# Performance work log

Hardware: AMD Instinct MI355X
Metric: run time of the kernel (lower is better)

The kernel has to match this reference:

```python
import jax, jax.numpy as jnp
import numpy as np

N_NODES = 50000
N_EDGES = 400000
D = 512
LN_EPS = 1e-5


def setup_inputs() -> dict:
    key = jax.random.key(0)
    k0, k1, k2, k3 = jax.random.split(key, 4)
    x = jax.random.normal(k0, (N_NODES, D), dtype=jnp.float32)
    src = jax.random.randint(k1, (N_EDGES,), 0, N_NODES, dtype=jnp.int64)
    dst = jax.random.randint(k2, (N_EDGES,), 0, N_NODES, dtype=jnp.int64)
    W = jax.random.normal(k3, (D, D), dtype=jnp.float32) * 0.05
    b = jnp.zeros((D,), dtype=jnp.float32)
    gamma = jnp.ones((D,), dtype=jnp.float32)
    beta = jnp.zeros((D,), dtype=jnp.float32)
    return {"x": x, "W": W, "b": b, "gamma": gamma, "beta": beta, "src": src, "dst": dst}


def reference(x, W, b, gamma, beta, src, dst):
    n = x.shape[0]
    ones = jnp.ones(src.shape, dtype=x.dtype)
    # DGL GraphConv norm='both': clamp degrees to >= 1
    deg_out = jnp.clip(jax.ops.segment_sum(ones, src, num_segments=n), 1.0)  # [N]
    deg_in = jnp.clip(jax.ops.segment_sum(ones, dst, num_segments=n), 1.0)   # [N]
    h = x * jax.lax.rsqrt(deg_out)[:, None]                 # [N, D] src normalization
    agg = jax.ops.segment_sum(h[src], dst, num_segments=n)  # gather->scatter-add SpMM
    h = agg * jax.lax.rsqrt(deg_in)[:, None]                # dst normalization
    h = h @ W + b                                           # dense linear
    # LayerNorm over last dim
    mu = jnp.mean(h, axis=-1, keepdims=True)
    var = jnp.mean(jnp.square(h - mu), axis=-1, keepdims=True)
    h = (h - mu) * jax.lax.rsqrt(var + LN_EPS) * gamma + beta
    # torch nn.GELU default = exact erf GELU
    return jax.nn.gelu(h, approximate=False)
```

## Files before the change

kernel.cpp:

```cpp
#include <hip/hip_runtime.h>
#include <hip/hip_bf16.h>

#define D 512

typedef __attribute__((ext_vector_type(8))) short bf16x8;
typedef __attribute__((ext_vector_type(4))) float f32x4;

__device__ inline float b2f(short h) {
    union { unsigned u; float f; } c;
    c.u = ((unsigned)(unsigned short)h) << 16;
    return c.f;
}

__global__ void k_hist(const int* __restrict__ src, const int* __restrict__ dst,
                       int* __restrict__ deg_out, int* __restrict__ deg_in, int E) {
    int e = blockIdx.x * 256 + threadIdx.x;
    if (e < E) {
        atomicAdd(&deg_out[src[e]], 1);
        atomicAdd(&deg_in[dst[e]], 1);
    }
}

__global__ __launch_bounds__(256)
void k_scale(const float* __restrict__ x, const int* __restrict__ deg_out,
             __hip_bfloat16* __restrict__ xs, int total16) {
    int i = blockIdx.x * 256 + threadIdx.x;
    if (i >= total16) return;
    int node = i >> 6;
    float w = rsqrtf((float)max(deg_out[node], 1));
    const float4* p = (const float4*)(x + (size_t)i * 8);
    float4 a = p[0], b = p[1];
    union { float4 f4; __hip_bfloat16 h[8]; } o;
    o.h[0] = __float2bfloat16(a.x * w);
    o.h[1] = __float2bfloat16(a.y * w);
    o.h[2] = __float2bfloat16(a.z * w);
    o.h[3] = __float2bfloat16(a.w * w);
    o.h[4] = __float2bfloat16(b.x * w);
    o.h[5] = __float2bfloat16(b.y * w);
    o.h[6] = __float2bfloat16(b.z * w);
    o.h[7] = __float2bfloat16(b.w * w);
    *(float4*)(xs + (size_t)i * 8) = o.f4;
}

__global__ void k_scan1(const int* __restrict__ deg_in, int* __restrict__ row_start,
                        int* __restrict__ partials, int N) {
    __shared__ int sm[1024];
    int tid = threadIdx.x;
    int i = blockIdx.x * 1024 + tid;
    int v = (i < N) ? deg_in[i] : 0;
    sm[tid] = v;
    __syncthreads();
    int acc = v;
    #pragma unroll
    for (int off = 1; off < 1024; off <<= 1) {
        int t = (tid >= off) ? sm[tid - off] : 0;
        __syncthreads();
        acc += t;
        sm[tid] = acc;
        __syncthreads();
    }
    if (i < N) row_start[i] = acc - v;
    if (tid == 1023) partials[blockIdx.x] = acc;
}

__global__ void k_scan2w(int* __restrict__ partials, int* __restrict__ row_start,
                         int nb, int N) {
    int lane = threadIdx.x;
    int orig = (lane < nb) ? partials[lane] : 0;
    int v = orig;
    #pragma unroll
    for (int off = 1; off < 64; off <<= 1) {
        int t = __shfl_up(v, off, 64);
        if (lane >= off) v += t;
    }
    if (lane < nb) partials[lane] = v - orig;
    if (lane == 63) row_start[N] = v;
}

__global__ void k_scan2s(int* __restrict__ partials, int* __restrict__ row_start,
                         int nb, int N) {
    if (threadIdx.x == 0 && blockIdx.x == 0) {
        int run = 0;
        for (int b = 0; b < nb; b++) { int t = partials[b]; partials[b] = run; run += t; }
        row_start[N] = run;
    }
}

__global__ void k_scan3(int* __restrict__ row_start, const int* __restrict__ partials, int N) {
    int i = blockIdx.x * 256 + threadIdx.x;
    if (i < N) row_start[i] += partials[i >> 10];
}

__global__ void k_fill(const int* __restrict__ src, const int* __restrict__ dst,
                       const int* __restrict__ row_start, int* __restrict__ cursor,
                       int* __restrict__ csr_src, int E) {
    int e = blockIdx.x * 256 + threadIdx.x;
    if (e < E) {
        int d = dst[e];
        int slot = atomicAdd(&cursor[d], 1);
        csr_src[row_start[d] + slot] = src[e];
    }
}

__global__ __launch_bounds__(1024)
void k_spmm(const __hip_bfloat16* __restrict__ xs, const int* __restrict__ row_start,
            const int* __restrict__ csr_src, __hip_bfloat16* __restrict__ Ap, int N) {
    int wid = threadIdx.x >> 6;
    int lane = threadIdx.x & 63;
    int node = blockIdx.x * 16 + wid;
    if (node >= N) return;
    int rs = row_start[node], re = row_start[node + 1];

    float acc[8];
    #pragma unroll
    for (int k = 0; k < 8; k++) acc[k] = 0.f;
    const __hip_bfloat16* xl = xs + (size_t)lane * 8;

    int j = rs;
    for (; j + 4 <= re; j += 4) {
        int s0 = csr_src[j], s1 = csr_src[j + 1], s2 = csr_src[j + 2], s3 = csr_src[j + 3];
        bf16x8 v0 = *(const bf16x8*)(xl + (size_t)s0 * D);
        bf16x8 v1 = *(const bf16x8*)(xl + (size_t)s1 * D);
        bf16x8 v2 = *(const bf16x8*)(xl + (size_t)s2 * D);
        bf16x8 v3 = *(const bf16x8*)(xl + (size_t)s3 * D);
        #pragma unroll
        for (int k = 0; k < 8; k++)
            acc[k] += (b2f(v0[k]) + b2f(v1[k])) + (b2f(v2[k]) + b2f(v3[k]));
    }
    for (; j < re; j++) {
        int s = csr_src[j];
        bf16x8 v = *(const bf16x8*)(xl + (size_t)s * D);
        #pragma unroll
        for (int k = 0; k < 8; k++) acc[k] += b2f(v[k]);
    }

    float rn = rsqrtf((float)max(re - rs, 1));
    union { float4 f4; __hip_bfloat16 h[8]; } o;
    #pragma unroll
    for (int k = 0; k < 8; k++) o.h[k] = __float2bfloat16(acc[k] * rn);
    *(float4*)((char*)Ap + ((size_t)(node >> 4) * 1024 + lane * 16 + (node & 15)) * 16) = o.f4;
}

__global__ __launch_bounds__(256)
void k_spmm_f32(const float* __restrict__ x, const int* __restrict__ row_start,
                const int* __restrict__ csr_src, const int* __restrict__ deg_out,
                __hip_bfloat16* __restrict__ A, int N) {
    int wid = threadIdx.x >> 6;
    int lane = threadIdx.x & 63;
    int node = blockIdx.x * 4 + wid;
    if (node >= N) return;
    int rs = row_start[node], re = row_start[node + 1];
    float4 acc0 = {0.f, 0.f, 0.f, 0.f};
    float4 acc1 = {0.f, 0.f, 0.f, 0.f};
    const float* xl = x + (size_t)lane * 8;
    for (int j = rs; j < re; j++) {
        int s = csr_src[j];
        float w = rsqrtf((float)max(deg_out[s], 1));
        const float4* p = (const float4*)(xl + (size_t)s * D);
        float4 a = p[0], b = p[1];
        acc0.x += a.x * w; acc0.y += a.y * w; acc0.z += a.z * w; acc0.w += a.w * w;
        acc1.x += b.x * w; acc1.y += b.y * w; acc1.z += b.z * w; acc1.w += b.w * w;
    }
    float rn = rsqrtf((float)max(re - rs, 1));
    union { float4 f4; __hip_bfloat16 h[8]; } o;
    o.h[0] = __float2bfloat16(acc0.x * rn);
    o.h[1] = __float2bfloat16(acc0.y * rn);
    o.h[2] = __float2bfloat16(acc0.z * rn);
    o.h[3] = __float2bfloat16(acc0.w * rn);
    o.h[4] = __float2bfloat16(acc1.x * rn);
    o.h[5] = __float2bfloat16(acc1.y * rn);
    o.h[6] = __float2bfloat16(acc1.z * rn);
    o.h[7] = __float2bfloat16(acc1.w * rn);
    *(float4*)(A + (size_t)node * D + lane * 8) = o.f4;
}

__global__ void k_packw2(const float* __restrict__ W, __hip_bfloat16* __restrict__ Wp) {
    int bid = blockIdx.x;
    int c = bid >> 7, kt = (bid >> 3) & 15, ntc = bid & 7;
    int lane = threadIdx.x;
    int k0 = kt * 32 + (lane >> 4) * 8;
    int n  = (c * 8 + ntc) * 16 + (lane & 15);
    union { float4 f4; __hip_bfloat16 h[8]; } o;
    #pragma unroll
    for (int j = 0; j < 8; j++)
        o.h[j] = __float2bfloat16(W[(size_t)(k0 + j) * D + n]);
    *(float4*)(Wp + ((size_t)bid * 64 + lane) * 8) = o.f4;
}

__global__ void k_packw(const float* __restrict__ W, __hip_bfloat16* __restrict__ Wp) {
    int tile = blockIdx.x;
    int lane = threadIdx.x;
    int kt = tile >> 5, nt = tile & 31;
    int k0 = kt * 32 + (lane >> 4) * 8;
    int n  = nt * 16 + (lane & 15);
    union { float4 f4; __hip_bfloat16 h[8]; } o;
    #pragma unroll
    for (int j = 0; j < 8; j++)
        o.h[j] = __float2bfloat16(W[(size_t)(k0 + j) * D + n]);
    *(float4*)(Wp + ((size_t)tile * 64 + lane) * 8) = o.f4;
}

__global__ __launch_bounds__(512, 4)
void k_gemm3(const __hip_bfloat16* __restrict__ Ap, const __hip_bfloat16* __restrict__ Wp,
             const float* __restrict__ bias, const float* __restrict__ gamma,
             const float* __restrict__ beta, float* __restrict__ out, int M) {
    __shared__ float s_sum[64][4];
    __shared__ float s_sq[64][4];

    int tid = threadIdx.x;
    int wid = tid >> 6, lane = tid & 63;
    int wm = wid >> 2, wn = wid & 3;
    int l4 = lane >> 4, coll = lane & 15;
    int tb = blockIdx.x * 64;
    int rgmax = ((M + 15) >> 4) - 1;

    int rg0 = (tb >> 4) + wm * 2;
    int rgA = min(rg0, rgmax);
    int rgB = min(rg0 + 1, rgmax);
    const char* a0 = (const char*)Ap + (size_t)rgA * 16384 + (size_t)lane * 16;
    const char* a1 = (const char*)Ap + (size_t)rgB * 16384 + (size_t)lane * 16;
    const char* wb = (const char*)Wp + ((size_t)(wn * 128) * 64 + lane) * 16;

    f32x4 acc0[8], acc1[8];
    #pragma unroll
    for (int t = 0; t < 8; t++) { acc0[t] = (f32x4){0,0,0,0}; acc1[t] = (f32x4){0,0,0,0}; }

    for (int kt = 0; kt < 16; kt++) {
        bf16x8 af0 = *(const bf16x8*)(a0 + (size_t)kt * 1024);
        bf16x8 af1 = *(const bf16x8*)(a1 + (size_t)kt * 1024);
        const char* wk = wb + (size_t)kt * 8192;
        #pragma unroll
        for (int t = 0; t < 8; t++) {
            bf16x8 bf = *(const bf16x8*)(wk + (size_t)t * 1024);
            acc0[t] = __builtin_amdgcn_mfma_f32_16x16x32_bf16(af0, bf, acc0[t], 0, 0, 0);
            acc1[t] = __builtin_amdgcn_mfma_f32_16x16x32_bf16(af1, bf, acc1[t], 0, 0, 0);
        }
    }

    float bia[8], gam[8], bet[8];
    #pragma unroll
    for (int t = 0; t < 8; t++) {
        int col = wn * 128 + t * 16 + coll;
        bia[t] = bias[col]; gam[t] = gamma[col]; bet[t] = beta[col];
    }
    #pragma unroll
    for (int ai = 0; ai < 2; ai++) {
        f32x4* acc = ai ? acc1 : acc0;
        #pragma unroll
        for (int r = 0; r < 4; r++) {
            float s = 0.f, q = 0.f;
            #pragma unroll
            for (int t = 0; t < 8; t++) {
                float v = acc[t][r] + bia[t];
                acc[t][r] = v;
                s += v; q += v * v;
            }
            #pragma unroll
            for (int off = 1; off < 16; off <<= 1) {
                s += __shfl_xor(s, off, 64);
                q += __shfl_xor(q, off, 64);
            }
            if (coll == 0) {
                int rb = wm * 32 + ai * 16 + l4 * 4 + r;
                s_sum[rb][wn] = s;
                s_sq[rb][wn] = q;
            }
        }
    }
    __syncthreads();

    #pragma unroll
    for (int ai = 0; ai < 2; ai++) {
        f32x4* acc = ai ? acc1 : acc0;
        #pragma unroll
        for (int r = 0; r < 4; r++) {
            int rb = wm * 32 + ai * 16 + l4 * 4 + r;
            int gr = tb + rb;
            if (gr >= M) continue;
            float s = s_sum[rb][0] + s_sum[rb][1] + s_sum[rb][2] + s_sum[rb][3];
            float q = s_sq[rb][0] + s_sq[rb][1] + s_sq[rb][2] + s_sq[rb][3];
            float mean = s * (1.0f / 512.0f);
            float var = q * (1.0f / 512.0f) - mean * mean;
            float rstd = rsqrtf(fmaxf(var, 0.f) + 1e-5f);
            float* orow = out + (size_t)gr * D + wn * 128 + coll;
            #pragma unroll
            for (int t = 0; t < 8; t++) {
                float y = (acc[t][r] - mean) * rstd * gam[t] + bet[t];
                float yy = y * y;
                float pz = fmaf(yy, -0.1029423374f, -2.3022076728f);
                float e = __builtin_amdgcn_exp2f(y * pz);
                float g = y * __builtin_amdgcn_rcpf(1.0f + e);
                orow[t * 16] = g;
            }
        }
    }
}

__global__ __launch_bounds__(512)
void k_gemm(const __hip_bfloat16* __restrict__ A, const __hip_bfloat16* __restrict__ Wp,
            const float* __restrict__ bias, const float* __restrict__ gamma,
            const float* __restrict__ beta, float* __restrict__ out, int M) {
    int tid = threadIdx.x;
    int wid = tid >> 6, lane = tid & 63;
    int wm = wid >> 2;
    int wn = wid & 3;
    int l4 = lane >> 4, coll = lane & 15;
    int m0 = blockIdx.x * 32 + wm * 16;
    int arow = m0 + coll;
    bool rowok = (arow < M);

    f32x4 acc[8];
    #pragma unroll
    for (int t = 0; t < 8; t++) acc[t] = (f32x4){0.f, 0.f, 0.f, 0.f};

    const bf16x8* wpb = (const bf16x8*)Wp;
    for (int kt = 0; kt < 16; kt++) {
        bf16x8 afrag;
        if (rowok) afrag = *(const bf16x8*)(A + (size_t)arow * D + kt * 32 + l4 * 8);
        else afrag = (bf16x8){0,0,0,0,0,0,0,0};
        const bf16x8* wp = wpb + ((size_t)(kt * 32 + wn * 8) * 64 + lane);
        #pragma unroll
        for (int t = 0; t < 8; t++) {
            bf16x8 bfrag = wp[(size_t)t * 64];
            acc[t] = __builtin_amdgcn_mfma_f32_16x16x32_bf16(afrag, bfrag, acc[t], 0, 0, 0);
        }
    }
    __shared__ float s_sum[32][4];
    __shared__ float s_sq[32][4];
    #pragma unroll
    for (int r = 0; r < 4; r++) {
        float s = 0.f, q = 0.f;
        #pragma unroll
        for (int t = 0; t < 8; t++) {
            int col = wn * 128 + t * 16 + coll;
            float v = acc[t][r] + bias[col];
            acc[t][r] = v;
            s += v; q += v * v;
        }
        #pragma unroll
        for (int off = 1; off < 16; off <<= 1) {
            s += __shfl_xor(s, off, 64);
            q += __shfl_xor(q, off, 64);
        }
        if (coll == 0) {
            int rb = wm * 16 + l4 * 4 + r;
            s_sum[rb][wn] = s;
            s_sq[rb][wn] = q;
        }
    }
    __syncthreads();
    #pragma unroll
    for (int r = 0; r < 4; r++) {
        int rb = wm * 16 + l4 * 4 + r;
        int gr = blockIdx.x * 32 + rb;
        if (gr >= M) continue;
        float s = s_sum[rb][0] + s_sum[rb][1] + s_sum[rb][2] + s_sum[rb][3];
        float q = s_sq[rb][0] + s_sq[rb][1] + s_sq[rb][2] + s_sq[rb][3];
        float mean = s * (1.0f / 512.0f);
        float var = q * (1.0f / 512.0f) - mean * mean;
        float rstd = rsqrtf(fmaxf(var, 0.f) + 1e-5f);
        #pragma unroll
        for (int t = 0; t < 8; t++) {
            int col = wn * 128 + t * 16 + coll;
            float y = (acc[t][r] - mean) * rstd * gamma[col] + beta[col];
            float yy = y * y;
            float pz = fmaf(yy, -0.1029423374f, -2.3022076728f);
            float e = __builtin_amdgcn_exp2f(y * pz);
            out[(size_t)gr * D + col] = y * __builtin_amdgcn_rcpf(1.0f + e);
        }
    }
}

extern "C" void kernel_launch(void* const* d_in, const int* in_sizes, int n_in,
                              void* d_out, int out_size, void* d_ws, size_t ws_size,
                              hipStream_t stream) {
    const float* x     = (const float*)d_in[0];
    const float* W     = (const float*)d_in[1];
    const float* b     = (const float*)d_in[2];
    const float* gamma = (const float*)d_in[3];
    const float* beta  = (const float*)d_in[4];
    const int*   src   = (const int*)d_in[5];
    const int*   dst   = (const int*)d_in[6];
    int N = in_sizes[0] / D;
    int E = in_sizes[5];
    float* out = (float*)d_out;

    int* deg_out   = (int*)d_ws;
    int* deg_in    = deg_out + N;
    int* row_start = deg_in + N;
    int* cursor    = row_start + N + 1;
    int* partials  = cursor + N;
    int* csr_src   = partials + 64;
    uintptr_t p = (uintptr_t)(csr_src + E);
    p = (p + 255) & ~(uintptr_t)255;
    __hip_bfloat16* A = (__hip_bfloat16*)p;
    p += (size_t)(((N + 15) / 16) * 16) * D * sizeof(__hip_bfloat16);
    p = (p + 255) & ~(uintptr_t)255;
    __hip_bfloat16* Wp = (__hip_bfloat16*)p;
    p += (size_t)D * D * sizeof(__hip_bfloat16);
    p = (p + 255) & ~(uintptr_t)255;
    __hip_bfloat16* xs = (__hip_bfloat16*)p;
    size_t need_xs = (p - (uintptr_t)d_ws) + (size_t)N * D * sizeof(__hip_bfloat16);
    bool use_bf16_path = (ws_size >= need_xs);

    hipMemsetAsync(deg_out, 0, (size_t)2 * N * sizeof(int), stream);
    hipMemsetAsync(cursor, 0, (size_t)N * sizeof(int), stream);

    k_hist<<<(E + 255) / 256, 256, 0, stream>>>(src, dst, deg_out, deg_in, E);
    int nb1 = (N + 1023) / 1024;
    k_scan1<<<nb1, 1024, 0, stream>>>(deg_in, row_start, partials, N);
    if (nb1 <= 64)
        k_scan2w<<<1, 64, 0, stream>>>(partials, row_start, nb1, N);
    else
        k_scan2s<<<1, 64, 0, stream>>>(partials, row_start, nb1, N);
    k_scan3<<<(N + 255) / 256, 256, 0, stream>>>(row_start, partials, N);
    k_fill<<<(E + 255) / 256, 256, 0, stream>>>(src, dst, row_start, cursor, csr_src, E);

    if (use_bf16_path) {
        int total16 = N * 64;
        k_scale<<<(total16 + 255) / 256, 256, 0, stream>>>(x, deg_out, xs, total16);
        k_spmm<<<(N + 15) / 16, 1024, 0, stream>>>(xs, row_start, csr_src, A, N);
        k_packw2<<<512, 64, 0, stream>>>(W, Wp);
        k_gemm3<<<(N + 63) / 64, 512, 0, stream>>>(A, Wp, b, gamma, beta, out, N);
    } else {
        k_spmm_f32<<<(N + 3) / 4, 256, 0, stream>>>(x, row_start, csr_src, deg_out, A, N);
        k_packw<<<512, 64, 0, stream>>>(W, Wp);
        k_gemm<<<(N + 31) / 32, 512, 0, stream>>>(A, Wp, b, gamma, beta, out, N);
    }
}
```

Baseline: 240.6 us.

## Use row-major A with 128-row GEMM tiles reusing W fragments across four row groups

The SpMM now writes the aggregated features row-major instead of in a packed 16-row MFMA layout, and runs with 256-thread blocks. The fused GEMM+LayerNorm+GELU kernel doubles its row tile to 128, so each wave holds four A fragments and reuses each loaded W fragment across four MFMAs, cutting W reloads per output. The cost is higher register pressure (occupancy hint dropped to 2), A loads that are strided by row rather than contiguous packed tiles, and fewer blocks in the grid.

```diff
diff --git a/kernel.cpp b/kernel.cpp
--- a/kernel.cpp
+++ b/kernel.cpp
@@ -102,12 +102,12 @@
     }
 }
 
-__global__ __launch_bounds__(1024)
+__global__ __launch_bounds__(256)
 void k_spmm(const __hip_bfloat16* __restrict__ xs, const int* __restrict__ row_start,
-            const int* __restrict__ csr_src, __hip_bfloat16* __restrict__ Ap, int N) {
+            const int* __restrict__ csr_src, __hip_bfloat16* __restrict__ A, int N) {
     int wid = threadIdx.x >> 6;
     int lane = threadIdx.x & 63;
-    int node = blockIdx.x * 16 + wid;
+    int node = blockIdx.x * 4 + wid;
     if (node >= N) return;
     int rs = row_start[node], re = row_start[node + 1];
 
@@ -138,7 +138,7 @@
     union { float4 f4; __hip_bfloat16 h[8]; } o;
     #pragma unroll
     for (int k = 0; k < 8; k++) o.h[k] = __float2bfloat16(acc[k] * rn);
-    *(float4*)((char*)Ap + ((size_t)(node >> 4) * 1024 + lane * 16 + (node & 15)) * 16) = o.f4;
+    *(float4*)(A + (size_t)node * D + lane * 8) = o.f4;
 }
 
 __global__ __launch_bounds__(256)
@@ -200,41 +200,49 @@
     *(float4*)(Wp + ((size_t)tile * 64 + lane) * 8) = o.f4;
 }
 
-__global__ __launch_bounds__(512, 4)
-void k_gemm3(const __hip_bfloat16* __restrict__ Ap, const __hip_bfloat16* __restrict__ Wp,
+__global__ __launch_bounds__(512, 2)
+void k_gemm4(const __hip_bfloat16* __restrict__ A, const __hip_bfloat16* __restrict__ Wp,
              const float* __restrict__ bias, const float* __restrict__ gamma,
              const float* __restrict__ beta, float* __restrict__ out, int M) {
-    __shared__ float s_sum[64][4];
-    __shared__ float s_sq[64][4];
+    __shared__ float s_sum[128][4];
+    __shared__ float s_sq[128][4];
 
     int tid = threadIdx.x;
     int wid = tid >> 6, lane = tid & 63;
     int wm = wid >> 2, wn = wid & 3;
     int l4 = lane >> 4, coll = lane & 15;
-    int tb = blockIdx.x * 64;
-    int rgmax = ((M + 15) >> 4) - 1;
-
-    int rg0 = (tb >> 4) + wm * 2;
-    int rgA = min(rg0, rgmax);
-    int rgB = min(rg0 + 1, rgmax);
-    const char* a0 = (const char*)Ap + (size_t)rgA * 16384 + (size_t)lane * 16;
-    const char* a1 = (const char*)Ap + (size_t)rgB * 16384 + (size_t)lane * 16;
+    int tb = blockIdx.x * 128;
+
+    const char* ap[4];
+    #pragma unroll
+    for (int ai = 0; ai < 4; ai++) {
+        int row = tb + wm * 64 + ai * 16 + coll;
+        if (row > M - 1) row = M - 1;
+        ap[ai] = (const char*)A + (size_t)row * 1024 + l4 * 16;
+    }
     const char* wb = (const char*)Wp + ((size_t)(wn * 128) * 64 + lane) * 16;
 
-    f32x4 acc0[8], acc1[8];
-    #pragma unroll
-    for (int t = 0; t < 8; t++) { acc0[t] = (f32x4){0,0,0,0}; acc1[t] = (f32x4){0,0,0,0}; }
+    f32x4 acc[4][8];
+    #pragma unroll
+    for (int ai = 0; ai < 4; ai++)
+        #pragma unroll
+        for (int t = 0; t < 8; t++) acc[ai][t] = (f32x4){0.f, 0.f, 0.f, 0.f};
 
     for (int kt = 0; kt < 16; kt++) {
-        bf16x8 af0 = *(const bf16x8*)(a0 + (size_t)kt * 1024);
-        bf16x8 af1 = *(const bf16x8*)(a1 + (size_t)kt * 1024);
+        bf16x8 af[4];
+        #pragma unroll
+        for (int ai = 0; ai < 4; ai++)
+            af[ai] = *(const bf16x8*)(ap[ai] + (size_t)kt * 64);
         const char* wk = wb + (size_t)kt * 8192;
-        #pragma unroll
-        for (int t = 0; t < 8; t++) {
-            bf16x8 bf = *(const bf16x8*)(wk + (size_t)t * 1024);
-            acc0[t] = __builtin_amdgcn_mfma_f32_16x16x32_bf16(af0, bf, acc0[t], 0, 0, 0);
-            acc1[t] = __builtin_amdgcn_mfma_f32_16x16x32_bf16(af1, bf, acc1[t], 0, 0, 0);
-        }
+        bf16x8 bf[8];
+        #pragma unroll
+        for (int t = 0; t < 8; t++)
+            bf[t] = *(const bf16x8*)(wk + (size_t)t * 1024);
+        #pragma unroll
+        for (int t = 0; t < 8; t++)
+            #pragma unroll
+            for (int ai = 0; ai < 4; ai++)
+                acc[ai][t] = __builtin_amdgcn_mfma_f32_16x16x32_bf16(af[ai], bf[t], acc[ai][t], 0, 0, 0);
     }
 
     float bia[8], gam[8], bet[8];
@@ -244,15 +252,14 @@
         bia[t] = bias[col]; gam[t] = gamma[col]; bet[t] = beta[col];
     }
     #pragma unroll
-    for (int ai = 0; ai < 2; ai++) {
-        f32x4* acc = ai ? acc1 : acc0;
+    for (int ai = 0; ai < 4; ai++) {
         #pragma unroll
         for (int r = 0; r < 4; r++) {
             float s = 0.f, q = 0.f;
             #pragma unroll
             for (int t = 0; t < 8; t++) {
-                float v = acc[t][r] + bia[t];
-                acc[t][r] = v;
+                float v = acc[ai][t][r] + bia[t];
+                acc[ai][t][r] = v;
                 s += v; q += v * v;
             }
             #pragma unroll
@@ -261,7 +268,7 @@
                 q += __shfl_xor(q, off, 64);
             }
             if (coll == 0) {
-                int rb = wm * 32 + ai * 16 + l4 * 4 + r;
+                int rb = wm * 64 + ai * 16 + l4 * 4 + r;
                 s_sum[rb][wn] = s;
                 s_sq[rb][wn] = q;
             }
@@ -270,11 +277,10 @@
     __syncthreads();
 
     #pragma unroll
-    for (int ai = 0; ai < 2; ai++) {
-        f32x4* acc = ai ? acc1 : acc0;
+    for (int ai = 0; ai < 4; ai++) {
         #pragma unroll
         for (int r = 0; r < 4; r++) {
-            int rb = wm * 32 + ai * 16 + l4 * 4 + r;
+            int rb = wm * 64 + ai * 16 + l4 * 4 + r;
             int gr = tb + rb;
             if (gr >= M) continue;
             float s = s_sum[rb][0] + s_sum[rb][1] + s_sum[rb][2] + s_sum[rb][3];
@@ -285,7 +291,7 @@
             float* orow = out + (size_t)gr * D + wn * 128 + coll;
             #pragma unroll
             for (int t = 0; t < 8; t++) {
-                float y = (acc[t][r] - mean) * rstd * gam[t] + bet[t];
+                float y = (acc[ai][t][r] - mean) * rstd * gam[t] + bet[t];
                 float yy = y * y;
                 float pz = fmaf(yy, -0.1029423374f, -2.3022076728f);
                 float e = __builtin_amdgcn_exp2f(y * pz);
@@ -394,7 +400,7 @@
     uintptr_t p = (uintptr_t)(csr_src + E);
     p = (p + 255) & ~(uintptr_t)255;
     __hip_bfloat16* A = (__hip_bfloat16*)p;
-    p += (size_t)(((N + 15) / 16) * 16) * D * sizeof(__hip_bfloat16);
+    p += (size_t)N * D * sizeof(__hip_bfloat16);
     p = (p + 255) & ~(uintptr_t)255;
     __hip_bfloat16* Wp = (__hip_bfloat16*)p;
     p += (size_t)D * D * sizeof(__hip_bfloat16);
@@ -419,9 +425,9 @@
     if (use_bf16_path) {
         int total16 = N * 64;
         k_scale<<<(total16 + 255) / 256, 256, 0, stream>>>(x, deg_out, xs, total16);
-        k_spmm<<<(N + 15) / 16, 1024, 0, stream>>>(xs, row_start, csr_src, A, N);
+        k_spmm<<<(N + 3) / 4, 256, 0, stream>>>(xs, row_start, csr_src, A, N);
         k_packw2<<<512, 64, 0, stream>>>(W, Wp);
-        k_gemm3<<<(N + 63) / 64, 512, 0, stream>>>(A, Wp, b, gamma, beta, out, N);
+        k_gemm4<<<(N + 127) / 128, 512, 0, stream>>>(A, Wp, b, gamma, beta, out, N);
     } else {
         k_spmm_f32<<<(N + 3) / 4, 256, 0, stream>>>(x, row_start, csr_src, deg_out, A, N);
         k_packw<<<512, 64, 0, stream>>>(W, Wp);
```

Measured after the change: 250.9 us. 4.3% more time.

## Fuse SpMM aggregation into GEMM+LayerNorm kernel via swizzled LDS tile

Applied to the files above, without the earlier changes.

The separate SpMM kernel is removed. Each GEMM block now gathers and aggregates its own 64 destination rows into a 64KB XOR-swizzled shared-memory tile, then runs the MFMA GEMM with the LayerNorm/GELU epilogue reading A from LDS. This avoids writing the aggregated bf16 matrix to global memory, reading it back, and paying one kernel launch. In exchange, 64KB of LDS per block caps occupancy at two blocks per CU, and the gather phase and MFMA phase can no longer overlap across kernels.

```diff
diff --git a/kernel.cpp b/kernel.cpp
--- a/kernel.cpp
+++ b/kernel.cpp
@@ -102,43 +102,152 @@
     }
 }
 
-__global__ __launch_bounds__(1024)
-void k_spmm(const __hip_bfloat16* __restrict__ xs, const int* __restrict__ row_start,
-            const int* __restrict__ csr_src, __hip_bfloat16* __restrict__ Ap, int N) {
-    int wid = threadIdx.x >> 6;
-    int lane = threadIdx.x & 63;
-    int node = blockIdx.x * 16 + wid;
-    if (node >= N) return;
-    int rs = row_start[node], re = row_start[node + 1];
-
-    float acc[8];
-    #pragma unroll
-    for (int k = 0; k < 8; k++) acc[k] = 0.f;
-    const __hip_bfloat16* xl = xs + (size_t)lane * 8;
-
-    int j = rs;
-    for (; j + 4 <= re; j += 4) {
-        int s0 = csr_src[j], s1 = csr_src[j + 1], s2 = csr_src[j + 2], s3 = csr_src[j + 3];
-        bf16x8 v0 = *(const bf16x8*)(xl + (size_t)s0 * D);
-        bf16x8 v1 = *(const bf16x8*)(xl + (size_t)s1 * D);
-        bf16x8 v2 = *(const bf16x8*)(xl + (size_t)s2 * D);
-        bf16x8 v3 = *(const bf16x8*)(xl + (size_t)s3 * D);
-        #pragma unroll
-        for (int k = 0; k < 8; k++)
-            acc[k] += (b2f(v0[k]) + b2f(v1[k])) + (b2f(v2[k]) + b2f(v3[k]));
-    }
-    for (; j < re; j++) {
-        int s = csr_src[j];
-        bf16x8 v = *(const bf16x8*)(xl + (size_t)s * D);
-        #pragma unroll
-        for (int k = 0; k < 8; k++) acc[k] += b2f(v[k]);
-    }
-
-    float rn = rsqrtf((float)max(re - rs, 1));
+__global__ void k_packw2(const float* __restrict__ W, __hip_bfloat16* __restrict__ Wp) {
+    int bid = blockIdx.x;
+    int c = bid >> 7, kt = (bid >> 3) & 15, ntc = bid & 7;
+    int lane = threadIdx.x;
+    int k0 = kt * 32 + (lane >> 4) * 8;
+    int n  = (c * 8 + ntc) * 16 + (lane & 15);
     union { float4 f4; __hip_bfloat16 h[8]; } o;
     #pragma unroll
-    for (int k = 0; k < 8; k++) o.h[k] = __float2bfloat16(acc[k] * rn);
-    *(float4*)((char*)Ap + ((size_t)(node >> 4) * 1024 + lane * 16 + (node & 15)) * 16) = o.f4;
+    for (int j = 0; j < 8; j++)
+        o.h[j] = __float2bfloat16(W[(size_t)(k0 + j) * D + n]);
+    *(float4*)(Wp + ((size_t)bid * 64 + lane) * 8) = o.f4;
+}
+
+__global__ __launch_bounds__(512, 2)
+void k_fused(const __hip_bfloat16* __restrict__ xs, const int* __restrict__ row_start,
+             const int* __restrict__ csr_src, const __hip_bfloat16* __restrict__ Wp,
+             const float* __restrict__ bias, const float* __restrict__ gamma,
+             const float* __restrict__ beta, float* __restrict__ out, int M) {
+    __shared__ __align__(16) char ldsA[65536];
+    __shared__ float s_sum[64][4];
+    __shared__ float s_sq[64][4];
+
+    int tid = threadIdx.x;
+    int wid = tid >> 6, lane = tid & 63;
+    int l4 = lane >> 4, coll = lane & 15;
+    int tb = blockIdx.x * 64;
+
+    {
+        const __hip_bfloat16* xl = xs + (size_t)lane * 8;
+        for (int i = 0; i < 8; i++) {
+            int rowt = wid * 8 + i;
+            int node = tb + rowt;
+            char* dst = ldsA + rowt * 1024 + ((lane * 16) ^ ((rowt & 7) << 4));
+            if (node < M) {
+                int rs = row_start[node], re = row_start[node + 1];
+                float acc[8];
+                #pragma unroll
+                for (int k = 0; k < 8; k++) acc[k] = 0.f;
+                int j = rs;
+                for (; j + 4 <= re; j += 4) {
+                    int s0 = csr_src[j], s1 = csr_src[j + 1], s2 = csr_src[j + 2], s3 = csr_src[j + 3];
+                    bf16x8 v0 = *(const bf16x8*)(xl + (size_t)s0 * D);
+                    bf16x8 v1 = *(const bf16x8*)(xl + (size_t)s1 * D);
+                    bf16x8 v2 = *(const bf16x8*)(xl + (size_t)s2 * D);
+                    bf16x8 v3 = *(const bf16x8*)(xl + (size_t)s3 * D);
+                    #pragma unroll
+                    for (int k = 0; k < 8; k++)
+                        acc[k] += (b2f(v0[k]) + b2f(v1[k])) + (b2f(v2[k]) + b2f(v3[k]));
+                }
+                for (; j < re; j++) {
+                    int s = csr_src[j];
+                    bf16x8 v = *(const bf16x8*)(xl + (size_t)s * D);
+                    #pragma unroll
+                    for (int k = 0; k < 8; k++) acc[k] += b2f(v[k]);
+                }
+                float rn = rsqrtf((float)max(re - rs, 1));
+                union { float4 f4; __hip_bfloat16 h[8]; } o;
+                #pragma unroll
+                for (int k = 0; k < 8; k++) o.h[k] = __float2bfloat16(acc[k] * rn);
+                *(float4*)dst = o.f4;
+            } else {
+                *(float4*)dst = (float4){0.f, 0.f, 0.f, 0.f};
+            }
+        }
+    }
+    __syncthreads();
+
+    int wm = wid >> 2, wn = wid & 3;
+    int r0 = wm * 32 + coll;
+    int r1 = r0 + 16;
+    const char* wb = (const char*)Wp + ((size_t)(wn * 128) * 64 + lane) * 16;
+
+    f32x4 acc0[8], acc1[8];
+    #pragma unroll
+    for (int t = 0; t < 8; t++) { acc0[t] = (f32x4){0,0,0,0}; acc1[t] = (f32x4){0,0,0,0}; }
+
+    for (int kt = 0; kt < 16; kt++) {
+        int kb = kt * 64 + l4 * 16;
+        bf16x8 af0 = *(const bf16x8*)(ldsA + r0 * 1024 + (kb ^ ((r0 & 7) << 4)));
+        bf16x8 af1 = *(const bf16x8*)(ldsA + r1 * 1024 + (kb ^ ((r1 & 7) << 4)));
+        const char* wk = wb + (size_t)kt * 8192;
+        #pragma unroll
+        for (int t = 0; t < 8; t++) {
+            bf16x8 bf = *(const bf16x8*)(wk + (size_t)t * 1024);
+            acc0[t] = __builtin_amdgcn_mfma_f32_16x16x32_bf16(af0, bf, acc0[t], 0, 0, 0);
+            acc1[t] = __builtin_amdgcn_mfma_f32_16x16x32_bf16(af1, bf, acc1[t], 0, 0, 0);
+        }
+    }
+
+    float bia[8], gam[8], bet[8];
+    #pragma unroll
+    for (int t = 0; t < 8; t++) {
+        int col = wn * 128 + t * 16 + coll;
+        bia[t] = bias[col]; gam[t] = gamma[col]; bet[t] = beta[col];
+    }
+    #pragma unroll
+    for (int ai = 0; ai < 2; ai++) {
+        f32x4* acc = ai ? acc1 : acc0;
+        #pragma unroll
+        for (int r = 0; r < 4; r++) {
+            float s = 0.f, q = 0.f;
+            #pragma unroll
+            for (int t = 0; t < 8; t++) {
+                float v = acc[t][r] + bia[t];
+                acc[t][r] = v;
+                s += v; q += v * v;
+            }
+            #pragma unroll
+            for (int off = 1; off < 16; off <<= 1) {
+                s += __shfl_xor(s, off, 64);
+                q += __shfl_xor(q, off, 64);
+            }
+            if (coll == 0) {
+                int rb = wm * 32 + ai * 16 + l4 * 4 + r;
+                s_sum[rb][wn] = s;
+                s_sq[rb][wn] = q;
+            }
+        }
+    }
+    __syncthreads();
+
+    #pragma unroll
+    for (int ai = 0; ai < 2; ai++) {
+        f32x4* acc = ai ? acc1 : acc0;
+        #pragma unroll
+        for (int r = 0; r < 4; r++) {
+            int rb = wm * 32 + ai * 16 + l4 * 4 + r;
+            int gr = tb + rb;
+            if (gr >= M) continue;
+            float s = s_sum[rb][0] + s_sum[rb][1] + s_sum[rb][2] + s_sum[rb][3];
+            float q = s_sq[rb][0] + s_sq[rb][1] + s_sq[rb][2] + s_sq[rb][3];
+            float mean = s * (1.0f / 512.0f);
+            float var = q * (1.0f / 512.0f) - mean * mean;
+            float rstd = rsqrtf(fmaxf(var, 0.f) + 1e-5f);
+            float* orow = out + (size_t)gr * D + wn * 128 + coll;
+            #pragma unroll
+            for (int t = 0; t < 8; t++) {
+                float y = (acc[t][r] - mean) * rstd * gam[t] + bet[t];
+                float yy = y * y;
+                float pz = fmaf(yy, -0.1029423374f, -2.3022076728f);
+                float e = __builtin_amdgcn_exp2f(y * pz);
+                float g = y * __builtin_amdgcn_rcpf(1.0f + e);
+                orow[t * 16] = g;
+            }
+        }
+    }
 }
 
 __global__ __launch_bounds__(256)
@@ -174,19 +283,6 @@
     *(float4*)(A + (size_t)node * D + lane * 8) = o.f4;
 }
 
-__global__ void k_packw2(const float* __restrict__ W, __hip_bfloat16* __restrict__ Wp) {
-    int bid = blockIdx.x;
-    int c = bid >> 7, kt = (bid >> 3) & 15, ntc = bid & 7;
-    int lane = threadIdx.x;
-    int k0 = kt * 32 + (lane >> 4) * 8;
-    int n  = (c * 8 + ntc) * 16 + (lane & 15);
-    union { float4 f4; __hip_bfloat16 h[8]; } o;
-    #pragma unroll
-    for (int j = 0; j < 8; j++)
-        o.h[j] = __float2bfloat16(W[(size_t)(k0 + j) * D + n]);
-    *(float4*)(Wp + ((size_t)bid * 64 + lane) * 8) = o.f4;
-}
-
 __global__ void k_packw(const float* __restrict__ W, __hip_bfloat16* __restrict__ Wp) {
     int tile = blockIdx.x;
     int lane = threadIdx.x;
@@ -198,102 +294,6 @@
     for (int j = 0; j < 8; j++)
         o.h[j] = __float2bfloat16(W[(size_t)(k0 + j) * D + n]);
     *(float4*)(Wp + ((size_t)tile * 64 + lane) * 8) = o.f4;
-}
-
-__global__ __launch_bounds__(512, 4)
-void k_gemm3(const __hip_bfloat16* __restrict__ Ap, const __hip_bfloat16* __restrict__ Wp,
-             const float* __restrict__ bias, const float* __restrict__ gamma,
-             const float* __restrict__ beta, float* __restrict__ out, int M) {
-    __shared__ float s_sum[64][4];
-    __shared__ float s_sq[64][4];
-
-    int tid = threadIdx.x;
-    int wid = tid >> 6, lane = tid & 63;
-    int wm = wid >> 2, wn = wid & 3;
-    int l4 = lane >> 4, coll = lane & 15;
-    int tb = blockIdx.x * 64;
-    int rgmax = ((M + 15) >> 4) - 1;
-
-    int rg0 = (tb >> 4) + wm * 2;
-    int rgA = min(rg0, rgmax);
-    int rgB = min(rg0 + 1, rgmax);
-    const char* a0 = (const char*)Ap + (size_t)rgA * 16384 + (size_t)lane * 16;
-    const char* a1 = (const char*)Ap + (size_t)rgB * 16384 + (size_t)lane * 16;
-    const char* wb = (const char*)Wp + ((size_t)(wn * 128) * 64 + lane) * 16;
-
-    f32x4 acc0[8], acc1[8];
-    #pragma unroll
-    for (int t = 0; t < 8; t++) { acc0[t] = (f32x4){0,0,0,0}; acc1[t] = (f32x4){0,0,0,0}; }
-
-    for (int kt = 0; kt < 16; kt++) {
-        bf16x8 af0 = *(const bf16x8*)(a0 + (size_t)kt * 1024);
-        bf16x8 af1 = *(const bf16x8*)(a1 + (size_t)kt * 1024);
-        const char* wk = wb + (size_t)kt * 8192;
-        #pragma unroll
-        for (int t = 0; t < 8; t++) {
-            bf16x8 bf = *(const bf16x8*)(wk + (size_t)t * 1024);
-            acc0[t] = __builtin_amdgcn_mfma_f32_16x16x32_bf16(af0, bf, acc0[t], 0, 0, 0);
-            acc1[t] = __builtin_amdgcn_mfma_f32_16x16x32_bf16(af1, bf, acc1[t], 0, 0, 0);
-        }
-    }
-
-    float bia[8], gam[8], bet[8];
-    #pragma unroll
-    for (int t = 0; t < 8; t++) {
-        int col = wn * 128 + t * 16 + coll;
-        bia[t] = bias[col]; gam[t] = gamma[col]; bet[t] = beta[col];
-    }
-    #pragma unroll
-    for (int ai = 0; ai < 2; ai++) {
-        f32x4* acc = ai ? acc1 : acc0;
-        #pragma unroll
-        for (int r = 0; r < 4; r++) {
-            float s = 0.f, q = 0.f;
-            #pragma unroll
-            for (int t = 0; t < 8; t++) {
-                float v = acc[t][r] + bia[t];
-                acc[t][r] = v;
-                s += v; q += v * v;
-            }
-            #pragma unroll
-            for (int off = 1; off < 16; off <<= 1) {
-                s += __shfl_xor(s, off, 64);
-                q += __shfl_xor(q, off, 64);
-            }
-            if (coll == 0) {
-                int rb = wm * 32 + ai * 16 + l4 * 4 + r;
-                s_sum[rb][wn] = s;
-                s_sq[rb][wn] = q;
-            }
-        }
-    }
-    __syncthreads();
-
-    #pragma unroll
-    for (int ai = 0; ai < 2; ai++) {
-        f32x4* acc = ai ? acc1 : acc0;
-        #pragma unroll
-        for (int r = 0; r < 4; r++) {
-            int rb = wm * 32 + ai * 16 + l4 * 4 + r;
-            int gr = tb + rb;
-            if (gr >= M) continue;
-            float s = s_sum[rb][0] + s_sum[rb][1] + s_sum[rb][2] + s_sum[rb][3];
-            float q = s_sq[rb][0] + s_sq[rb][1] + s_sq[rb][2] + s_sq[rb][3];
-            float mean = s * (1.0f / 512.0f);
-            float var = q * (1.0f / 512.0f) - mean * mean;
-            float rstd = rsqrtf(fmaxf(var, 0.f) + 1e-5f);
-            float* orow = out + (size_t)gr * D + wn * 128 + coll;
-            #pragma unroll
-            for (int t = 0; t < 8; t++) {
-                float y = (acc[t][r] - mean) * rstd * gam[t] + bet[t];
-                float yy = y * y;
-                float pz = fmaf(yy, -0.1029423374f, -2.3022076728f);
-                float e = __builtin_amdgcn_exp2f(y * pz);
-                float g = y * __builtin_amdgcn_rcpf(1.0f + e);
-                orow[t * 16] = g;
-            }
-        }
-    }
 }
 
 __global__ __launch_bounds__(512)
@@ -394,7 +394,7 @@
     uintptr_t p = (uintptr_t)(csr_src + E);
     p = (p + 255) & ~(uintptr_t)255;
     __hip_bfloat16* A = (__hip_bfloat16*)p;
-    p += (size_t)(((N + 15) / 16) * 16) * D * sizeof(__hip_bfloat16);
+    p += (size_t)N * D * sizeof(__hip_bfloat16);
     p = (p + 255) & ~(uintptr_t)255;
     __hip_bfloat16* Wp = (__hip_bfloat16*)p;
     p += (size_t)D * D * sizeof(__hip_bfloat16);
@@ -419,9 +419,9 @@
     if (use_bf16_path) {
         int total16 = N * 64;
         k_scale<<<(total16 + 255) / 256, 256, 0, stream>>>(x, deg_out, xs, total16);
-        k_spmm<<<(N + 15) / 16, 1024, 0, stream>>>(xs, row_start, csr_src, A, N);
         k_packw2<<<512, 64, 0, stream>>>(W, Wp);
-        k_gemm3<<<(N + 63) / 64, 512, 0, stream>>>(A, Wp, b, gamma, beta, out, N);
+        k_fused<<<(N + 63) / 64, 512, 0, stream>>>(xs, row_start, csr_src, Wp,
+                                                   b, gamma, beta, out, N);
     } else {
         k_spmm_f32<<<(N + 3) / 4, 256, 0, stream>>>(x, row_start, csr_src, deg_out, A, N);
         k_packw<<<512, 64, 0, stream>>>(W, Wp);
```

After: 291.4 us. 21.1% more time.

## Fuse degree scan with x scaling and seed cursor with row offsets

Applied to the files above, without the earlier changes.

Replaces the three-stage multi-kernel prefix scan with a single-block scan that runs in block 0 of a new kernel, while the remaining 256 blocks scale x to bf16 in a grid-stride loop. The cursor array is initialised to the row offsets, so the fill kernel writes directly to the atomic slot and the separate cursor memset and row_start read are dropped. This removes several launches and a memset. In exchange the scan is serialised in one block, which may become the critical path, and the scale pass now runs on fewer blocks.

```diff
diff --git a/kernel.cpp b/kernel.cpp
--- a/kernel.cpp
+++ b/kernel.cpp
@@ -21,84 +21,70 @@
     }
 }
 
-__global__ __launch_bounds__(256)
-void k_scale(const float* __restrict__ x, const int* __restrict__ deg_out,
-             __hip_bfloat16* __restrict__ xs, int total16) {
-    int i = blockIdx.x * 256 + threadIdx.x;
-    if (i >= total16) return;
-    int node = i >> 6;
-    float w = rsqrtf((float)max(deg_out[node], 1));
-    const float4* p = (const float4*)(x + (size_t)i * 8);
-    float4 a = p[0], b = p[1];
-    union { float4 f4; __hip_bfloat16 h[8]; } o;
-    o.h[0] = __float2bfloat16(a.x * w);
-    o.h[1] = __float2bfloat16(a.y * w);
-    o.h[2] = __float2bfloat16(a.z * w);
-    o.h[3] = __float2bfloat16(a.w * w);
-    o.h[4] = __float2bfloat16(b.x * w);
-    o.h[5] = __float2bfloat16(b.y * w);
-    o.h[6] = __float2bfloat16(b.z * w);
-    o.h[7] = __float2bfloat16(b.w * w);
-    *(float4*)(xs + (size_t)i * 8) = o.f4;
-}
-
-__global__ void k_scan1(const int* __restrict__ deg_in, int* __restrict__ row_start,
-                        int* __restrict__ partials, int N) {
-    __shared__ int sm[1024];
-    int tid = threadIdx.x;
-    int i = blockIdx.x * 1024 + tid;
-    int v = (i < N) ? deg_in[i] : 0;
-    sm[tid] = v;
-    __syncthreads();
-    int acc = v;
-    #pragma unroll
-    for (int off = 1; off < 1024; off <<= 1) {
-        int t = (tid >= off) ? sm[tid - off] : 0;
+__global__ __launch_bounds__(1024)
+void k_scale_scan(const float* __restrict__ x, const int* __restrict__ deg_out,
+                  const int* __restrict__ deg_in, __hip_bfloat16* __restrict__ xs,
+                  int* __restrict__ row_start, int* __restrict__ cursor,
+                  int N, int total16, int do_scale) {
+    if (blockIdx.x == 0) {
+        __shared__ int sm[1024];
+        int tid = threadIdx.x;
+        int per = (N + 1023) >> 10;
+        int base = tid * per;
+        int local = 0;
+        for (int i = 0; i < per; i++) {
+            int idx = base + i;
+            if (idx < N) local += deg_in[idx];
+        }
+        sm[tid] = local;
         __syncthreads();
-        acc += t;
-        sm[tid] = acc;
-        __syncthreads();
-    }
-    if (i < N) row_start[i] = acc - v;
-    if (tid == 1023) partials[blockIdx.x] = acc;
-}
-
-__global__ void k_scan2w(int* __restrict__ partials, int* __restrict__ row_start,
-                         int nb, int N) {
-    int lane = threadIdx.x;
-    int orig = (lane < nb) ? partials[lane] : 0;
-    int v = orig;
-    #pragma unroll
-    for (int off = 1; off < 64; off <<= 1) {
-        int t = __shfl_up(v, off, 64);
-        if (lane >= off) v += t;
-    }
-    if (lane < nb) partials[lane] = v - orig;
-    if (lane == 63) row_start[N] = v;
-}
-
-__global__ void k_scan2s(int* __restrict__ partials, int* __restrict__ row_start,
-                         int nb, int N) {
-    if (threadIdx.x == 0 && blockIdx.x == 0) {
-        int run = 0;
-        for (int b = 0; b < nb; b++) { int t = partials[b]; partials[b] = run; run += t; }
-        row_start[N] = run;
-    }
-}
-
-__global__ void k_scan3(int* __restrict__ row_start, const int* __restrict__ partials, int N) {
-    int i = blockIdx.x * 256 + threadIdx.x;
-    if (i < N) row_start[i] += partials[i >> 10];
+        int acc = local;
+        #pragma unroll
+        for (int off = 1; off < 1024; off <<= 1) {
+            int t = (tid >= off) ? sm[tid - off] : 0;
+            __syncthreads();
+            acc += t;
+            sm[tid] = acc;
+            __syncthreads();
+        }
+        int run = acc - local;
+        for (int i = 0; i < per; i++) {
+            int idx = base + i;
+            if (idx < N) {
+                row_start[idx] = run;
+                cursor[idx] = run;
+                run += deg_in[idx];
+            }
+        }
+        if (tid == 1023) row_start[N] = run;
+        return;
+    }
+    if (!do_scale) return;
+    int stride = (gridDim.x - 1) * 1024;
+    for (int i = (blockIdx.x - 1) * 1024 + threadIdx.x; i < total16; i += stride) {
+        int node = i >> 6;
+        float w = rsqrtf((float)max(deg_out[node], 1));
+        const float4* p = (const float4*)(x + (size_t)i * 8);
+        float4 a = p[0], b = p[1];
+        union { float4 f4; __hip_bfloat16 h[8]; } o;
+        o.h[0] = __float2bfloat16(a.x * w);
+        o.h[1] = __float2bfloat16(a.y * w);
+        o.h[2] = __float2bfloat16(a.z * w);
+        o.h[3] = __float2bfloat16(a.w * w);
+        o.h[4] = __float2bfloat16(b.x * w);
+        o.h[5] = __float2bfloat16(b.y * w);
+        o.h[6] = __float2bfloat16(b.z * w);
+        o.h[7] = __float2bfloat16(b.w * w);
+        *(float4*)(xs + (size_t)i * 8) = o.f4;
+    }
 }
 
 __global__ void k_fill(const int* __restrict__ src, const int* __restrict__ dst,
-                       const int* __restrict__ row_start, int* __restrict__ cursor,
-                       int* __restrict__ csr_src, int E) {
+                       int* __restrict__ cursor, int* __restrict__ csr_src, int E) {
     int e = blockIdx.x * 256 + threadIdx.x;
     if (e < E) {
-        int d = dst[e];
-        int slot = atomicAdd(&cursor[d], 1);
-        csr_src[row_start[d] + slot] = src[e];
+        int slot = atomicAdd(&cursor[dst[e]], 1);
+        csr_src[slot] = src[e];
     }
 }
 
@@ -139,6 +125,115 @@
     #pragma unroll
     for (int k = 0; k < 8; k++) o.h[k] = __float2bfloat16(acc[k] * rn);
     *(float4*)((char*)Ap + ((size_t)(node >> 4) * 1024 + lane * 16 + (node & 15)) * 16) = o.f4;
+}
+
+__global__ void k_packw2(const float* __restrict__ W, __hip_bfloat16* __restrict__ Wp) {
+    int bid = blockIdx.x;
+    int c = bid >> 7, kt = (bid >> 3) & 15, ntc = bid & 7;
+    int lane = threadIdx.x;
+    int k0 = kt * 32 + (lane >> 4) * 8;
+    int n  = (c * 8 + ntc) * 16 + (lane & 15);
+    union { float4 f4; __hip_bfloat16 h[8]; } o;
+    #pragma unroll
+    for (int j = 0; j < 8; j++)
+        o.h[j] = __float2bfloat16(W[(size_t)(k0 + j) * D + n]);
+    *(float4*)(Wp + ((size_t)bid * 64 + lane) * 8) = o.f4;
+}
+
+__global__ __launch_bounds__(512, 4)
+void k_gemm3(const __hip_bfloat16* __restrict__ Ap, const __hip_bfloat16* __restrict__ Wp,
+             const float* __restrict__ bias, const float* __restrict__ gamma,
+             const float* __restrict__ beta, float* __restrict__ out, int M) {
+    __shared__ float s_sum[64][4];
+    __shared__ float s_sq[64][4];
+
+    int tid = threadIdx.x;
+    int wid = tid >> 6, lane = tid & 63;
+    int wm = wid >> 2, wn = wid & 3;
+    int l4 = lane >> 4, coll = lane & 15;
+    int tb = blockIdx.x * 64;
+    int rgmax = ((M + 15) >> 4) - 1;
+
+    int rg0 = (tb >> 4) + wm * 2;
+    int rgA = min(rg0, rgmax);
+    int rgB = min(rg0 + 1, rgmax);
+    const char* a0 = (const char*)Ap + (size_t)rgA * 16384 + (size_t)lane * 16;
+    const char* a1 = (const char*)Ap + (size_t)rgB * 16384 + (size_t)lane * 16;
+    const char* wb = (const char*)Wp + ((size_t)(wn * 128) * 64 + lane) * 16;
+
+    f32x4 acc0[8], acc1[8];
+    #pragma unroll
+    for (int t = 0; t < 8; t++) { acc0[t] = (f32x4){0,0,0,0}; acc1[t] = (f32x4){0,0,0,0}; }
+
+    for (int kt = 0; kt < 16; kt++) {
+        bf16x8 af0 = *(const bf16x8*)(a0 + (size_t)kt * 1024);
+        bf16x8 af1 = *(const bf16x8*)(a1 + (size_t)kt * 1024);
+        const char* wk = wb + (size_t)kt * 8192;
+        #pragma unroll
+        for (int t = 0; t < 8; t++) {
+            bf16x8 bf = *(const bf16x8*)(wk + (size_t)t * 1024);
+            acc0[t] = __builtin_amdgcn_mfma_f32_16x16x32_bf16(af0, bf, acc0[t], 0, 0, 0);
+            acc1[t] = __builtin_amdgcn_mfma_f32_16x16x32_bf16(af1, bf, acc1[t], 0, 0, 0);
+        }
+    }
+
+    float bia[8], gam[8], bet[8];
+    #pragma unroll
+    for (int t = 0; t < 8; t++) {
+        int col = wn * 128 + t * 16 + coll;
+        bia[t] = bias[col]; gam[t] = gamma[col]; bet[t] = beta[col];
+    }
+    #pragma unroll
+    for (int ai = 0; ai < 2; ai++) {
+        f32x4* acc = ai ? acc1 : acc0;
+        #pragma unroll
+        for (int r = 0; r < 4; r++) {
+            float s = 0.f, q = 0.f;
+            #pragma unroll
+            for (int t = 0; t < 8; t++) {
+                float v = acc[t][r] + bia[t];
+                acc[t][r] = v;
+                s += v; q += v * v;
+            }
+            #pragma unroll
+            for (int off = 1; off < 16; off <<= 1) {
+                s += __shfl_xor(s, off, 64);
+                q += __shfl_xor(q, off, 64);
+            }
+            if (coll == 0) {
+                int rb = wm * 32 + ai * 16 + l4 * 4 + r;
+                s_sum[rb][wn] = s;
+                s_sq[rb][wn] = q;
+            }
+        }
+    }
+    __syncthreads();
+
+    #pragma unroll
+    for (int ai = 0; ai < 2; ai++) {
+        f32x4* acc = ai ? acc1 : acc0;
+        #pragma unroll
+        for (int r = 0; r < 4; r++) {
+            int rb = wm * 32 + ai * 16 + l4 * 4 + r;
+            int gr = tb + rb;
+            if (gr >= M) continue;
+            float s = s_sum[rb][0] + s_sum[rb][1] + s_sum[rb][2] + s_sum[rb][3];
+            float q = s_sq[rb][0] + s_sq[rb][1] + s_sq[rb][2] + s_sq[rb][3];
+            float mean = s * (1.0f / 512.0f);
+            float var = q * (1.0f / 512.0f) - mean * mean;
+            float rstd = rsqrtf(fmaxf(var, 0.f) + 1e-5f);
+            float* orow = out + (size_t)gr * D + wn * 128 + coll;
+            #pragma unroll
+            for (int t = 0; t < 8; t++) {
+                float y = (acc[t][r] - mean) * rstd * gam[t] + bet[t];
+                float yy = y * y;
+                float pz = fmaf(yy, -0.1029423374f, -2.3022076728f);
+                float e = __builtin_amdgcn_exp2f(y * pz);
+                float g = y * __builtin_amdgcn_rcpf(1.0f + e);
+                orow[t * 16] = g;
+            }
+        }
+    }
 }
 
 __global__ __launch_bounds__(256)
@@ -174,19 +269,6 @@
     *(float4*)(A + (size_t)node * D + lane * 8) = o.f4;
 }
 
-__global__ void k_packw2(const float* __restrict__ W, __hip_bfloat16* __restrict__ Wp) {
-    int bid = blockIdx.x;
-    int c = bid >> 7, kt = (bid >> 3) & 15, ntc = bid & 7;
-    int lane = threadIdx.x;
-    int k0 = kt * 32 + (lane >> 4) * 8;
-    int n  = (c * 8 + ntc) * 16 + (lane & 15);
-    union { float4 f4; __hip_bfloat16 h[8]; } o;
-    #pragma unroll
-    for (int j = 0; j < 8; j++)
-        o.h[j] = __float2bfloat16(W[(size_t)(k0 + j) * D + n]);
-    *(float4*)(Wp + ((size_t)bid * 64 + lane) * 8) = o.f4;
-}
-
 __global__ void k_packw(const float* __restrict__ W, __hip_bfloat16* __restrict__ Wp) {
     int tile = blockIdx.x;
     int lane = threadIdx.x;
@@ -198,102 +280,6 @@
     for (int j = 0; j < 8; j++)
         o.h[j] = __float2bfloat16(W[(size_t)(k0 + j) * D + n]);
     *(float4*)(Wp + ((size_t)tile * 64 + lane) * 8) = o.f4;
-}
-
-__global__ __launch_bounds__(512, 4)
-void k_gemm3(const __hip_bfloat16* __restrict__ Ap, const __hip_bfloat16* __restrict__ Wp,
-             const float* __restrict__ bias, const float* __restrict__ gamma,
-             const float* __restrict__ beta, float* __restrict__ out, int M) {
-    __shared__ float s_sum[64][4];
-    __shared__ float s_sq[64][4];
-
-    int tid = threadIdx.x;
-    int wid = tid >> 6, lane = tid & 63;
-    int wm = wid >> 2, wn = wid & 3;
-    int l4 = lane >> 4, coll = lane & 15;
-    int tb = blockIdx.x * 64;
-    int rgmax = ((M + 15) >> 4) - 1;
-
-    int rg0 = (tb >> 4) + wm * 2;
-    int rgA = min(rg0, rgmax);
-    int rgB = min(rg0 + 1, rgmax);
-    const char* a0 = (const char*)Ap + (size_t)rgA * 16384 + (size_t)lane * 16;
-    const char* a1 = (const char*)Ap + (size_t)rgB * 16384 + (size_t)lane * 16;
-    const char* wb = (const char*)Wp + ((size_t)(wn * 128) * 64 + lane) * 16;
-
-    f32x4 acc0[8], acc1[8];
-    #pragma unroll
-    for (int t = 0; t < 8; t++) { acc0[t] = (f32x4){0,0,0,0}; acc1[t] = (f32x4){0,0,0,0}; }
-
-    for (int kt = 0; kt < 16; kt++) {
-        bf16x8 af0 = *(const bf16x8*)(a0 + (size_t)kt * 1024);
-        bf16x8 af1 = *(const bf16x8*)(a1 + (size_t)kt * 1024);
-        const char* wk = wb + (size_t)kt * 8192;
-        #pragma unroll
-        for (int t = 0; t < 8; t++) {
-            bf16x8 bf = *(const bf16x8*)(wk + (size_t)t * 1024);
-            acc0[t] = __builtin_amdgcn_mfma_f32_16x16x32_bf16(af0, bf, acc0[t], 0, 0, 0);
-            acc1[t] = __builtin_amdgcn_mfma_f32_16x16x32_bf16(af1, bf, acc1[t], 0, 0, 0);
-        }
-    }
-
-    float bia[8], gam[8], bet[8];
-    #pragma unroll
-    for (int t = 0; t < 8; t++) {
-        int col = wn * 128 + t * 16 + coll;
-        bia[t] = bias[col]; gam[t] = gamma[col]; bet[t] = beta[col];
-    }
-    #pragma unroll
-    for (int ai = 0; ai < 2; ai++) {
-        f32x4* acc = ai ? acc1 : acc0;
-        #pragma unroll
-        for (int r = 0; r < 4; r++) {
-            float s = 0.f, q = 0.f;
-            #pragma unroll
-            for (int t = 0; t < 8; t++) {
-                float v = acc[t][r] + bia[t];
-                acc[t][r] = v;
-                s += v; q += v * v;
-            }
-            #pragma unroll
-            for (int off = 1; off < 16; off <<= 1) {
-                s += __shfl_xor(s, off, 64);
-                q += __shfl_xor(q, off, 64);
-            }
-            if (coll == 0) {
-                int rb = wm * 32 + ai * 16 + l4 * 4 + r;
-                s_sum[rb][wn] = s;
-                s_sq[rb][wn] = q;
-            }
-        }
-    }
-    __syncthreads();
-
-    #pragma unroll
-    for (int ai = 0; ai < 2; ai++) {
-        f32x4* acc = ai ? acc1 : acc0;
-        #pragma unroll
-        for (int r = 0; r < 4; r++) {
-            int rb = wm * 32 + ai * 16 + l4 * 4 + r;
-            int gr = tb + rb;
-            if (gr >= M) continue;
-            float s = s_sum[rb][0] + s_sum[rb][1] + s_sum[rb][2] + s_sum[rb][3];
-            float q = s_sq[rb][0] + s_sq[rb][1] + s_sq[rb][2] + s_sq[rb][3];
-            float mean = s * (1.0f / 512.0f);
-            float var = q * (1.0f / 512.0f) - mean * mean;
-            float rstd = rsqrtf(fmaxf(var, 0.f) + 1e-5f);
-            float* orow = out + (size_t)gr * D + wn * 128 + coll;
-            #pragma unroll
-            for (int t = 0; t < 8; t++) {
-                float y = (acc[t][r] - mean) * rstd * gam[t] + bet[t];
-                float yy = y * y;
-                float pz = fmaf(yy, -0.1029423374f, -2.3022076728f);
-                float e = __builtin_amdgcn_exp2f(y * pz);
-                float g = y * __builtin_amdgcn_rcpf(1.0f + e);
-                orow[t * 16] = g;
-            }
-        }
-    }
 }
 
 __global__ __launch_bounds__(512)
@@ -389,11 +375,10 @@
     int* deg_in    = deg_out + N;
     int* row_start = deg_in + N;
     int* cursor    = row_start + N + 1;
-    int* partials  = cursor + N;
-    int* csr_src   = partials + 64;
+    int* csr_src   = cursor + N;
     uintptr_t p = (uintptr_t)(csr_src + E);
     p = (p + 255) & ~(uintptr_t)255;
-    __hip_bfloat16* A = (__hip_bfloat16*)p;
+    __hip_bfloat16* Ap = (__hip_bfloat16*)p;
     p += (size_t)(((N + 15) / 16) * 16) * D * sizeof(__hip_bfloat16);
     p = (p + 255) & ~(uintptr_t)255;
     __hip_bfloat16* Wp = (__hip_bfloat16*)p;
@@ -401,30 +386,23 @@
     p = (p + 255) & ~(uintptr_t)255;
     __hip_bfloat16* xs = (__hip_bfloat16*)p;
     size_t need_xs = (p - (uintptr_t)d_ws) + (size_t)N * D * sizeof(__hip_bfloat16);
-    bool use_bf16_path = (ws_size >= need_xs);
+    bool main_path = (ws_size >= need_xs);
 
     hipMemsetAsync(deg_out, 0, (size_t)2 * N * sizeof(int), stream);
-    hipMemsetAsync(cursor, 0, (size_t)N * sizeof(int), stream);
 
     k_hist<<<(E + 255) / 256, 256, 0, stream>>>(src, dst, deg_out, deg_in, E);
-    int nb1 = (N + 1023) / 1024;
-    k_scan1<<<nb1, 1024, 0, stream>>>(deg_in, row_start, partials, N);
-    if (nb1 <= 64)
-        k_scan2w<<<1, 64, 0, stream>>>(partials, row_start, nb1, N);
-    else
-        k_scan2s<<<1, 64, 0, stream>>>(partials, row_start, nb1, N);
-    k_scan3<<<(N + 255) / 256, 256, 0, stream>>>(row_start, partials, N);
-    k_fill<<<(E + 255) / 256, 256, 0, stream>>>(src, dst, row_start, cursor, csr_src, E);
-
-    if (use_bf16_path) {
-        int total16 = N * 64;
-        k_scale<<<(total16 + 255) / 256, 256, 0, stream>>>(x, deg_out, xs, total16);
-        k_spmm<<<(N + 15) / 16, 1024, 0, stream>>>(xs, row_start, csr_src, A, N);
+    int total16 = N * 64;
+    k_scale_scan<<<257, 1024, 0, stream>>>(x, deg_out, deg_in, xs, row_start, cursor,
+                                           N, total16, main_path ? 1 : 0);
+    k_fill<<<(E + 255) / 256, 256, 0, stream>>>(src, dst, cursor, csr_src, E);
+
+    if (main_path) {
+        k_spmm<<<(N + 15) / 16, 1024, 0, stream>>>(xs, row_start, csr_src, Ap, N);
         k_packw2<<<512, 64, 0, stream>>>(W, Wp);
-        k_gemm3<<<(N + 63) / 64, 512, 0, stream>>>(A, Wp, b, gamma, beta, out, N);
+        k_gemm3<<<(N + 63) / 64, 512, 0, stream>>>(Ap, Wp, b, gamma, beta, out, N);
     } else {
-        k_spmm_f32<<<(N + 3) / 4, 256, 0, stream>>>(x, row_start, csr_src, deg_out, A, N);
+        k_spmm_f32<<<(N + 3) / 4, 256, 0, stream>>>(x, row_start, csr_src, deg_out, Ap, N);
         k_packw<<<512, 64, 0, stream>>>(W, Wp);
-        k_gemm<<<(N + 31) / 32, 512, 0, stream>>>(A, Wp, b, gamma, beta, out, N);
-    }
-}
+        k_gemm<<<(N + 31) / 32, 512, 0, stream>>>(Ap, Wp, b, gamma, beta, out, N);
+    }
+}
```

New measurement: 367.6 us. 52.8% more time.
